# Kernel optimization log

Hardware: AMD Instinct MI355X
Metric: run time of the kernel (lower is better)

## Reference

```python
import jax, jax.numpy as jnp
import numpy as np

B, L, DIM, HEADS, DIM_HEAD = 16, 1024, 512, 8, 64


def _make_perms(rng):
    # perm = identity on first DIM indices, random permutation of [DIM, L*DIM) after
    perms = []
    for _ in range(HEADS - 1):
        tail = rng.permutation(np.arange(DIM, L * DIM))
        perms.append(np.concatenate([np.arange(DIM), tail]))
    return jnp.asarray(np.stack(perms), dtype=jnp.int64)


def setup_inputs() -> dict:
    key = jax.random.key(0)
    ks = jax.random.split(key, 6)
    s = 0.02
    return {
        "x": jax.random.normal(ks[0], (B, L, DIM), dtype=jnp.float32),
        "perms": _make_perms(np.random.default_rng(0)),
        "Wq": jax.random.normal(ks[1], (HEADS, DIM, DIM_HEAD), dtype=jnp.float32) * s,
        "Wk": jax.random.normal(ks[2], (HEADS, DIM, DIM_HEAD), dtype=jnp.float32) * s,
        "Wv": jax.random.normal(ks[3], (HEADS, DIM, DIM_HEAD), dtype=jnp.float32) * s,
        "Wo": jax.random.normal(ks[4], (DIM, HEADS * DIM_HEAD), dtype=jnp.float32) * s,
        "bo": jnp.zeros((DIM,), dtype=jnp.float32),
    }


def reference(x, perms, Wq, Wk, Wv, Wo, bo):
    b, l, d = x.shape
    h, _, e = Wq.shape
    scale = e ** -0.5
    # shuffled query inputs for heads 1..h-1
    flat = x.reshape(b, l * d)                      # [B, L*D]
    shuf = flat[:, perms].reshape(b, h - 1, l, d)   # [B, H-1, L, D]
    xq = jnp.concatenate([x[:, None], shuf], axis=1)  # [B, H, L, D]
    q = jnp.einsum('bhld,hde->bhle', xq, Wq)
    k = jnp.einsum('bld,hde->bhle', x, Wk)
    v = jnp.einsum('bld,hde->bhle', x, Wv)
    attn = jax.nn.softmax(jnp.einsum('bhqe,bhke->bhqk', q, k) * scale, axis=-1)
    out = jnp.einsum('bhqk,bhke->bhqe', attn, v)    # [B, H, L, E]
    out = out.transpose(0, 2, 1, 3).reshape(b, l, h * e)  # concat heads on last dim
    return jnp.einsum('bli,di->bld', out, Wo) + bo
```

## Files before the change

kernel.cpp:

```cpp
#include <hip/hip_runtime.h>

#define LL 1024
#define DD 512
#define HH 8
#define EE 64
#define LDX (LL*DD)
#define BB 16

typedef _Float16 h8 __attribute__((ext_vector_type(8)));
typedef _Float16 h4 __attribute__((ext_vector_type(4)));
typedef float f4 __attribute__((ext_vector_type(4)));
typedef int i4 __attribute__((ext_vector_type(4)));

__device__ __forceinline__ f4 mfma16(h8 a, h8 b, f4 c) {
    return __builtin_amdgcn_mfma_f32_16x16x32_f16(a, b, c, 0, 0, 0);
}

__global__ __launch_bounds__(256) void k_prep(
    const float* __restrict__ x, _Float16* __restrict__ xT)
{
    const int s = blockIdx.x * 256 + threadIdx.x;
    h8 lo, hi;
    #pragma unroll
    for (int b = 0; b < 8; ++b)  lo[b] = (_Float16)x[(size_t)b*LDX + s];
    #pragma unroll
    for (int b = 0; b < 8; ++b)  hi[b] = (_Float16)x[(size_t)(b+8)*LDX + s];
    _Float16* d = xT + (size_t)s * BB;
    *(h8*)d = lo; *(h8*)(d + 8) = hi;
}

__global__ __launch_bounds__(256) void k_x16(
    const float* __restrict__ x, _Float16* __restrict__ x16)
{
    const int i = blockIdx.x * 256 + threadIdx.x;
    f4 v = ((const f4*)x)[i];
    h4 o;
    #pragma unroll
    for (int j = 0; j < 4; ++j) o[j] = (_Float16)v[j];
    *(h4*)(x16 + 4*(size_t)i) = o;
}

__global__ __launch_bounds__(256) void k_wprep(
    const float* __restrict__ Wq, const float* __restrict__ Wk,
    const float* __restrict__ Wv, _Float16* __restrict__ WT)
{
    const int d0 = blockIdx.x * 64;
    const int zz = blockIdx.y;
    const float* src; float sc = 1.f;
    if (zz < 8)       src = Wk + (size_t)zz*DD*EE;
    else if (zz < 16) src = Wv + (size_t)(zz-8)*DD*EE;
    else            { src = Wq + (size_t)(zz-16)*DD*EE; sc = 0.125f; }
    const int t = threadIdx.x;
    const int e = t & 63, dq = t >> 6;
    #pragma unroll
    for (int i = 0; i < 16; ++i) {
        int d = d0 + dq*16 + i;
        WT[(size_t)(zz*64 + e)*DD + d] = (_Float16)(src[(size_t)d*EE + e] * sc);
    }
}

__global__ __launch_bounds__(256) void k_wo16(
    const float* __restrict__ Wo, _Float16* __restrict__ Wo16)
{
    const int i = blockIdx.x * 256 + threadIdx.x;
    f4 v = ((const f4*)Wo)[i];
    #pragma unroll
    for (int j = 0; j < 4; ++j) Wo16[4*i + j] = (_Float16)v[j];
}

__global__ __launch_bounds__(256) void k_qkv(
    const _Float16* __restrict__ x16, const _Float16* __restrict__ WT,
    _Float16* __restrict__ qw, _Float16* __restrict__ kw, _Float16* __restrict__ vw)
{
    const int y  = blockIdx.x;
    const int r0 = blockIdx.y * 128;

    __shared__ __align__(16) _Float16 As[2][128][72];
    __shared__ __align__(16) _Float16 Bs[2][128][72];

    const int t = threadIdx.x;
    const int wv = t >> 6, lane = t & 63;
    const int m = lane & 15, qd = lane >> 4;
    const int sr = t >> 1, sc0 = (t & 1) * 32;

    const _Float16* ax = x16 + (size_t)(r0 + sr)*DD + sc0;
    const _Float16* bx = WT  + (size_t)(y*128 + sr)*DD + sc0;

    #pragma unroll
    for (int c = 0; c < 4; ++c) {
        *(h8*)&As[0][sr][sc0 + 8*c] = *(const h8*)(ax + 8*c);
        *(h8*)&Bs[0][sr][sc0 + 8*c] = *(const h8*)(bx + 8*c);
    }
    __syncthreads();

    f4 acc[2][8] = {};
    int cur = 0;
    for (int kt = 0; kt < 8; ++kt) {
        const int alt = cur ^ 1;
        h8 an[4], bn[4];
        if (kt < 7) {
            const _Float16* a2 = ax + (kt+1)*64;
            const _Float16* b2 = bx + (kt+1)*64;
            #pragma unroll
            for (int c = 0; c < 4; ++c) {
                an[c] = *(const h8*)(a2 + 8*c);
                bn[c] = *(const h8*)(b2 + 8*c);
            }
        }
        #pragma unroll
        for (int ks = 0; ks < 2; ++ks) {
            h8 a0 = *(const h8*)&As[cur][32*wv +  0 + m][32*ks + 8*qd];
            h8 a1 = *(const h8*)&As[cur][32*wv + 16 + m][32*ks + 8*qd];
            #pragma unroll
            for (int nt = 0; nt < 8; ++nt) {
                h8 bb = *(const h8*)&Bs[cur][16*nt + m][32*ks + 8*qd];
                acc[0][nt] = mfma16(a0, bb, acc[0][nt]);
                acc[1][nt] = mfma16(a1, bb, acc[1][nt]);
            }
        }
        if (kt < 7) {
            #pragma unroll
            for (int c = 0; c < 4; ++c) {
                *(h8*)&As[alt][sr][sc0 + 8*c] = an[c];
                *(h8*)&Bs[alt][sr][sc0 + 8*c] = bn[c];
            }
            __syncthreads();
            cur = alt;
        }
    }

    #pragma unroll
    for (int nt = 0; nt < 8; ++nt) {
        const int n = y*128 + 16*nt + m;
        const int z = n >> 6, e = n & 63;
        if (z >= 17) continue;
        _Float16* dst; int h;
        if (z < 8)       { dst = kw; h = z; }
        else if (z < 16) { dst = vw; h = z - 8; }
        else             { dst = qw; h = 0; }
        dst += (size_t)h*LL*EE + e;
        #pragma unroll
        for (int mt = 0; mt < 2; ++mt)
            #pragma unroll
            for (int r = 0; r < 4; ++r) {
                int R = r0 + 32*wv + 16*mt + 4*qd + r;
                int b = R >> 10, l = R & 1023;
                dst[((size_t)b*HH*LL + l)*EE] = (_Float16)acc[mt][nt][r];
            }
    }
}

__global__ __launch_bounds__(256) void k_qshuf(
    const _Float16* __restrict__ xT, const int* __restrict__ perms,
    const _Float16* __restrict__ WT, _Float16* __restrict__ qw)
{
    const int l0 = blockIdx.x * 4;
    const int h  = blockIdx.y + 1;
    const _Float16* Wb = WT + (size_t)((16 + h)*64)*DD;
    const int* pbase = perms + (size_t)(h-1)*LDX;

    __shared__ __align__(16) _Float16 As[2][64][72];
    __shared__ __align__(16) _Float16 Bs[2][64][72];

    const int t = threadIdx.x;
    const int wv = t >> 6, lane = t & 63;
    const int m = lane & 15, qd = lane >> 4;
    const int lg = t >> 6, kcol = t & 63;
    const int br = t >> 2, bc0 = (t & 3) * 16;

    int pv[8];
    #pragma unroll
    for (int kt = 0; kt < 8; ++kt)
        pv[kt] = pbase[(size_t)(l0 + lg)*DD + kt*64 + kcol];

    {
        const _Float16* g = xT + (size_t)pv[0] * BB;
        h8 g0 = *(const h8*)g, g1 = *(const h8*)(g + 8);
        const _Float16* s = Wb + (size_t)br*DD + bc0;
        *(h8*)&Bs[0][br][bc0]     = *(const h8*)s;
        *(h8*)&Bs[0][br][bc0 + 8] = *(const h8*)(s + 8);
        #pragma unroll
        for (int i = 0; i < 8; ++i) As[0][lg*16 + i][kcol]     = g0[i];
        #pragma unroll
        for (int i = 0; i < 8; ++i) As[0][lg*16 + 8 + i][kcol] = g1[i];
    }
    __syncthreads();

    f4 acc[4] = {};
    int cur = 0;
    for (int kt = 0; kt < 8; ++kt) {
        const int alt = cur ^ 1;
        h8 g0n, g1n, b0n, b1n;
        if (kt < 7) {
            const _Float16* g = xT + (size_t)pv[kt+1] * BB;
            g0n = *(const h8*)g; g1n = *(const h8*)(g + 8);
            const _Float16* s = Wb + (size_t)br*DD + (kt+1)*64 + bc0;
            b0n = *(const h8*)s; b1n = *(const h8*)(s + 8);
        }
        #pragma unroll
        for (int ks = 0; ks < 2; ++ks) {
            h8 a = *(const h8*)&As[cur][16*wv + m][32*ks + 8*qd];
            #pragma unroll
            for (int nt = 0; nt < 4; ++nt) {
                h8 bb = *(const h8*)&Bs[cur][16*nt + m][32*ks + 8*qd];
                acc[nt] = mfma16(a, bb, acc[nt]);
            }
        }
        if (kt < 7) {
            *(h8*)&Bs[alt][br][bc0]     = b0n;
            *(h8*)&Bs[alt][br][bc0 + 8] = b1n;
            #pragma unroll
            for (int i = 0; i < 8; ++i) As[alt][lg*16 + i][kcol]     = g0n[i];
            #pragma unroll
            for (int i = 0; i < 8; ++i) As[alt][lg*16 + 8 + i][kcol] = g1n[i];
            __syncthreads();
            cur = alt;
        }
    }
    #pragma unroll
    for (int nt = 0; nt < 4; ++nt)
        #pragma unroll
        for (int r = 0; r < 4; ++r) {
            int b = 4*qd + r;
            qw[((size_t)(b*HH + h)*LL + l0 + wv)*EE + 16*nt + m] = (_Float16)acc[nt][r];
        }
}

__global__ __launch_bounds__(256, 3) void k_attn(
    const _Float16* __restrict__ qw, const _Float16* __restrict__ kw,
    const _Float16* __restrict__ vw, _Float16* __restrict__ oa)
{
    const int bh = blockIdx.x;
    const int l0 = blockIdx.y * 128;
    const int b = bh >> 3, h = bh & 7;
    const _Float16* qb = qw + ((size_t)bh*LL + l0)*EE;
    const _Float16* kb = kw + (size_t)bh*LL*EE;
    const _Float16* vb = vw + (size_t)bh*LL*EE;

    __shared__ __align__(16) _Float16 KsF[2][64*64];
    __shared__ __align__(16) _Float16 VtsF[2][64*64];
    __shared__ __align__(16) _Float16 Ps[128][72];

    const int t = threadIdx.x;
    const int wv = t >> 6, lane = t & 63;
    const int m = lane & 15, qd = lane >> 4;
    const int m7 = m & 7;
    const int krow = t >> 2, c0 = t & 3;
    const int vkey = t & 63, vec = t >> 6;
    const int vhi = vkey >> 3, vlo = vkey & 7;

    h8 qa[2][2];
    #pragma unroll
    for (int mt = 0; mt < 2; ++mt)
        #pragma unroll
        for (int ks = 0; ks < 2; ++ks)
            qa[mt][ks] = *(const h8*)(qb + (size_t)(32*wv + 16*mt + m)*EE + 32*ks + 8*qd);

    f4 oacc[2][4] = {};
    float lp[2][4] = {};

    {
        const _Float16* sk = kb + (size_t)krow*EE + 16*c0;
        h8 k0 = *(const h8*)sk, k1 = *(const h8*)(sk + 8);
        const _Float16* sv = vb + (size_t)vkey*EE + 16*vec;
        h8 v0 = *(const h8*)sv, v1 = *(const h8*)(sv + 8);
        *(h8*)&KsF[0][(krow<<6) + 8*((2*c0)     ^ (krow & 7))] = k0;
        *(h8*)&KsF[0][(krow<<6) + 8*((2*c0 + 1) ^ (krow & 7))] = k1;
        #pragma unroll
        for (int i = 0; i < 8; ++i)
            VtsF[0][((16*vec + i)<<6)     + 8*(vhi ^ i) + vlo] = v0[i];
        #pragma unroll
        for (int i = 0; i < 8; ++i)
            VtsF[0][((16*vec + 8 + i)<<6) + 8*(vhi ^ i) + vlo] = v1[i];
    }
    __syncthreads();

    for (int kt = 0; kt < 16; ++kt) {
        const int cur = kt & 1, alt = cur ^ 1;
        h8 kn0, kn1, vn0, vn1;
        if (kt < 15) {
            const _Float16* sk = kb + (size_t)((kt+1)*64 + krow)*EE + 16*c0;
            kn0 = *(const h8*)sk; kn1 = *(const h8*)(sk + 8);
            const _Float16* sv = vb + (size_t)((kt+1)*64 + vkey)*EE + 16*vec;
            vn0 = *(const h8*)sv; vn1 = *(const h8*)(sv + 8);
        }
        f4 sacc[2][4] = {};
        #pragma unroll
        for (int ks = 0; ks < 2; ++ks)
            #pragma unroll
            for (int nt = 0; nt < 4; ++nt) {
                h8 kf = *(const h8*)&KsF[cur][((16*nt + m)<<6) + 8*((4*ks + qd) ^ m7)];
                sacc[0][nt] = mfma16(qa[0][ks], kf, sacc[0][nt]);
                sacc[1][nt] = mfma16(qa[1][ks], kf, sacc[1][nt]);
            }
        #pragma unroll
        for (int mt = 0; mt < 2; ++mt)
            #pragma unroll
            for (int nt = 0; nt < 4; ++nt)
                #pragma unroll
                for (int r = 0; r < 4; ++r) {
                    float e = __expf(sacc[mt][nt][r]);
                    lp[mt][r] += e;
                    Ps[32*wv + 16*mt + 4*qd + r][16*nt + m] = (_Float16)e;
                }
        #pragma unroll
        for (int ks = 0; ks < 2; ++ks) {
            h8 pa0 = *(const h8*)&Ps[32*wv +  0 + m][32*ks + 8*qd];
            h8 pa1 = *(const h8*)&Ps[32*wv + 16 + m][32*ks + 8*qd];
            #pragma unroll
            for (int nt = 0; nt < 4; ++nt) {
                h8 vf = *(const h8*)&VtsF[cur][((16*nt + m)<<6) + 8*((4*ks + qd) ^ m7)];
                oacc[0][nt] = mfma16(pa0, vf, oacc[0][nt]);
                oacc[1][nt] = mfma16(pa1, vf, oacc[1][nt]);
            }
        }
        if (kt < 15) {
            *(h8*)&KsF[alt][(krow<<6) + 8*((2*c0)     ^ (krow & 7))] = kn0;
            *(h8*)&KsF[alt][(krow<<6) + 8*((2*c0 + 1) ^ (krow & 7))] = kn1;
            #pragma unroll
            for (int i = 0; i < 8; ++i)
                VtsF[alt][((16*vec + i)<<6)     + 8*(vhi ^ i) + vlo] = vn0[i];
            #pragma unroll
            for (int i = 0; i < 8; ++i)
                VtsF[alt][((16*vec + 8 + i)<<6) + 8*(vhi ^ i) + vlo] = vn1[i];
            __syncthreads();
        }
    }

    #pragma unroll
    for (int mt = 0; mt < 2; ++mt)
        #pragma unroll
        for (int r = 0; r < 4; ++r) {
            float s = lp[mt][r];
            s += __shfl_xor(s, 1, 64);
            s += __shfl_xor(s, 2, 64);
            s += __shfl_xor(s, 4, 64);
            s += __shfl_xor(s, 8, 64);
            lp[mt][r] = s;
        }

    _Float16* ob = oa + ((size_t)(b*LL + l0))*(HH*EE) + h*EE;
    #pragma unroll
    for (int mt = 0; mt < 2; ++mt)
        #pragma unroll
        for (int nt = 0; nt < 4; ++nt)
            #pragma unroll
            for (int r = 0; r < 4; ++r) {
                int row = 32*wv + 16*mt + 4*qd + r;
                ob[(size_t)row*(HH*EE) + 16*nt + m] = (_Float16)(oacc[mt][nt][r] / lp[mt][r]);
            }
}

__global__ __launch_bounds__(256) void k_oproj(
    const _Float16* __restrict__ oa, const _Float16* __restrict__ Wo16,
    const float* __restrict__ bo, float* __restrict__ out)
{
    const int y  = blockIdx.x;
    const int r0 = blockIdx.y * 128;

    __shared__ __align__(16) _Float16 As[2][128][72];
    __shared__ __align__(16) _Float16 Bs[2][128][72];

    const int t = threadIdx.x;
    const int wv = t >> 6, lane = t & 63;
    const int m = lane & 15, qd = lane >> 4;
    const int sr = t >> 1, sc0 = (t & 1) * 32;

    const _Float16* ax = oa   + (size_t)(r0 + sr)*DD + sc0;
    const _Float16* bx = Wo16 + (size_t)(y*128 + sr)*DD + sc0;

    #pragma unroll
    for (int c = 0; c < 4; ++c) {
        *(h8*)&As[0][sr][sc0 + 8*c] = *(const h8*)(ax + 8*c);
        *(h8*)&Bs[0][sr][sc0 + 8*c] = *(const h8*)(bx + 8*c);
    }
    __syncthreads();

    f4 acc[2][8] = {};
    int cur = 0;
    for (int kt = 0; kt < 8; ++kt) {
        const int alt = cur ^ 1;
        h8 an[4], bn[4];
        if (kt < 7) {
            const _Float16* a2 = ax + (kt+1)*64;
            const _Float16* b2 = bx + (kt+1)*64;
            #pragma unroll
            for (int c = 0; c < 4; ++c) {
                an[c] = *(const h8*)(a2 + 8*c);
                bn[c] = *(const h8*)(b2 + 8*c);
            }
        }
        #pragma unroll
        for (int ks = 0; ks < 2; ++ks) {
            h8 a0 = *(const h8*)&As[cur][32*wv +  0 + m][32*ks + 8*qd];
            h8 a1 = *(const h8*)&As[cur][32*wv + 16 + m][32*ks + 8*qd];
            #pragma unroll
            for (int nt = 0; nt < 8; ++nt) {
                h8 bb = *(const h8*)&Bs[cur][16*nt + m][32*ks + 8*qd];
                acc[0][nt] = mfma16(a0, bb, acc[0][nt]);
                acc[1][nt] = mfma16(a1, bb, acc[1][nt]);
            }
        }
        if (kt < 7) {
            #pragma unroll
            for (int c = 0; c < 4; ++c) {
                *(h8*)&As[alt][sr][sc0 + 8*c] = an[c];
                *(h8*)&Bs[alt][sr][sc0 + 8*c] = bn[c];
            }
            __syncthreads();
            cur = alt;
        }
    }

    #pragma unroll
    for (int nt = 0; nt < 8; ++nt) {
        const int col = y*128 + 16*nt + m;
        const float bias = bo[col];
        #pragma unroll
        for (int mt = 0; mt < 2; ++mt)
            #pragma unroll
            for (int r = 0; r < 4; ++r) {
                int row = 32*wv + 16*mt + 4*qd + r;
                out[(size_t)(r0 + row)*DD + col] = acc[mt][nt][r] + bias;
            }
    }
}

extern "C" void kernel_launch(void* const* d_in, const int* in_sizes, int n_in,
                              void* d_out, int out_size, void* d_ws, size_t ws_size,
                              hipStream_t stream)
{
    const float* x  = (const float*)d_in[0];
    const int*   pm = (const int*)d_in[1];
    const float* Wq = (const float*)d_in[2];
    const float* Wk = (const float*)d_in[3];
    const float* Wv = (const float*)d_in[4];
    const float* Wo = (const float*)d_in[5];
    const float* bo = (const float*)d_in[6];
    float* out = (float*)d_out;

    const size_t QS = (size_t)BB * HH * LL * EE;
    _Float16* q    = (_Float16*)d_ws;
    _Float16* k    = q + QS;
    _Float16* v    = k + QS;
    _Float16* oaw  = v + QS;
    _Float16* xT   = oaw;
    _Float16* WT   = oaw + QS;
    _Float16* Wo16 = WT + (size_t)24*64*DD;
    _Float16* x16  = (_Float16*)d_out;

    k_x16  <<<dim3(LDX*BB/1024),    256, 0, stream>>>(x, x16);
    k_prep <<<dim3(LDX/256),        256, 0, stream>>>(x, xT);
    k_wprep<<<dim3(8, 24),          256, 0, stream>>>(Wq, Wk, Wv, WT);
    k_wo16 <<<dim3(DD*DD/1024),     256, 0, stream>>>(Wo, Wo16);
    k_qkv  <<<dim3(9, BB*LL/128),   256, 0, stream>>>(x16, WT, q, k, v);
    k_qshuf<<<dim3(LL/4, HH-1),     256, 0, stream>>>(xT, pm, WT, q);
    k_attn <<<dim3(BB*HH, LL/128),  256, 0, stream>>>(q, k, v, oaw);
    k_oproj<<<dim3(DD/128, BB*LL/128), 256, 0, stream>>>(oaw, Wo16, bo, out);
}
```

Before: 290.4 us.

## Use exp2 with folded log2e scale, MFMA row sums, prefetch all gathered rows

Folds log2(e) into the Q weight scale so the attention kernel can use the hardware exp2 directly. The softmax row sums are now computed by extra MFMAs against a ones vector instead of per-element VALU adds and shuffle reductions, and the final division becomes a multiply by the reciprocal. In the Q-projection kernel, all eight gathered xT rows are loaded up front to expose more memory parallelism, at the cost of more registers. The row sums now accumulate from fp16-rounded probabilities rather than fp32 values.

```diff
diff --git a/kernel.cpp b/kernel.cpp
--- a/kernel.cpp
+++ b/kernel.cpp
@@ -49,7 +49,7 @@
     const float* src; float sc = 1.f;
     if (zz < 8)       src = Wk + (size_t)zz*DD*EE;
     else if (zz < 16) src = Wv + (size_t)(zz-8)*DD*EE;
-    else            { src = Wq + (size_t)(zz-16)*DD*EE; sc = 0.125f; }
+    else            { src = Wq + (size_t)(zz-16)*DD*EE; sc = 0.18033688011112042f; }
     const int t = threadIdx.x;
     const int e = t & 63, dq = t >> 6;
     #pragma unroll
@@ -173,16 +173,22 @@
     for (int kt = 0; kt < 8; ++kt)
         pv[kt] = pbase[(size_t)(l0 + lg)*DD + kt*64 + kcol];
 
+    h8 g0[8], g1[8];
+    #pragma unroll
+    for (int kt = 0; kt < 8; ++kt) {
+        const _Float16* g = xT + (size_t)pv[kt] * BB;
+        g0[kt] = *(const h8*)g;
+        g1[kt] = *(const h8*)(g + 8);
+    }
+
     {
-        const _Float16* g = xT + (size_t)pv[0] * BB;
-        h8 g0 = *(const h8*)g, g1 = *(const h8*)(g + 8);
         const _Float16* s = Wb + (size_t)br*DD + bc0;
         *(h8*)&Bs[0][br][bc0]     = *(const h8*)s;
         *(h8*)&Bs[0][br][bc0 + 8] = *(const h8*)(s + 8);
         #pragma unroll
-        for (int i = 0; i < 8; ++i) As[0][lg*16 + i][kcol]     = g0[i];
-        #pragma unroll
-        for (int i = 0; i < 8; ++i) As[0][lg*16 + 8 + i][kcol] = g1[i];
+        for (int i = 0; i < 8; ++i) As[0][lg*16 + i][kcol]     = g0[0][i];
+        #pragma unroll
+        for (int i = 0; i < 8; ++i) As[0][lg*16 + 8 + i][kcol] = g1[0][i];
     }
     __syncthreads();
 
@@ -190,10 +196,8 @@
     int cur = 0;
     for (int kt = 0; kt < 8; ++kt) {
         const int alt = cur ^ 1;
-        h8 g0n, g1n, b0n, b1n;
-        if (kt < 7) {
-            const _Float16* g = xT + (size_t)pv[kt+1] * BB;
-            g0n = *(const h8*)g; g1n = *(const h8*)(g + 8);
+        h8 b0n, b1n;
+        if (kt < 7) {
             const _Float16* s = Wb + (size_t)br*DD + (kt+1)*64 + bc0;
             b0n = *(const h8*)s; b1n = *(const h8*)(s + 8);
         }
@@ -210,9 +214,9 @@
             *(h8*)&Bs[alt][br][bc0]     = b0n;
             *(h8*)&Bs[alt][br][bc0 + 8] = b1n;
             #pragma unroll
-            for (int i = 0; i < 8; ++i) As[alt][lg*16 + i][kcol]     = g0n[i];
-            #pragma unroll
-            for (int i = 0; i < 8; ++i) As[alt][lg*16 + 8 + i][kcol] = g1n[i];
+            for (int i = 0; i < 8; ++i) As[alt][lg*16 + i][kcol]     = g0[kt+1][i];
+            #pragma unroll
+            for (int i = 0; i < 8; ++i) As[alt][lg*16 + 8 + i][kcol] = g1[kt+1][i];
             __syncthreads();
             cur = alt;
         }
@@ -256,8 +260,14 @@
         for (int ks = 0; ks < 2; ++ks)
             qa[mt][ks] = *(const h8*)(qb + (size_t)(32*wv + 16*mt + m)*EE + 32*ks + 8*qd);
 
+    h8 bones = {};
+    if (m == 0) {
+        #pragma unroll
+        for (int i = 0; i < 8; ++i) bones[i] = (_Float16)1.0f;
+    }
+
     f4 oacc[2][4] = {};
-    float lp[2][4] = {};
+    f4 lsacc[2] = {};
 
     {
         const _Float16* sk = kb + (size_t)krow*EE + 16*c0;
@@ -298,11 +308,9 @@
             #pragma unroll
             for (int nt = 0; nt < 4; ++nt)
                 #pragma unroll
-                for (int r = 0; r < 4; ++r) {
-                    float e = __expf(sacc[mt][nt][r]);
-                    lp[mt][r] += e;
-                    Ps[32*wv + 16*mt + 4*qd + r][16*nt + m] = (_Float16)e;
-                }
+                for (int r = 0; r < 4; ++r)
+                    Ps[32*wv + 16*mt + 4*qd + r][16*nt + m] =
+                        (_Float16)__builtin_amdgcn_exp2f(sacc[mt][nt][r]);
         #pragma unroll
         for (int ks = 0; ks < 2; ++ks) {
             h8 pa0 = *(const h8*)&Ps[32*wv +  0 + m][32*ks + 8*qd];
@@ -313,6 +321,8 @@
                 oacc[0][nt] = mfma16(pa0, vf, oacc[0][nt]);
                 oacc[1][nt] = mfma16(pa1, vf, oacc[1][nt]);
             }
+            lsacc[0] = mfma16(pa0, bones, lsacc[0]);
+            lsacc[1] = mfma16(pa1, bones, lsacc[1]);
         }
         if (kt < 15) {
             *(h8*)&KsF[alt][(krow<<6) + 8*((2*c0)     ^ (krow & 7))] = kn0;
@@ -327,17 +337,12 @@
         }
     }
 
+    float inv[2][4];
     #pragma unroll
     for (int mt = 0; mt < 2; ++mt)
         #pragma unroll
-        for (int r = 0; r < 4; ++r) {
-            float s = lp[mt][r];
-            s += __shfl_xor(s, 1, 64);
-            s += __shfl_xor(s, 2, 64);
-            s += __shfl_xor(s, 4, 64);
-            s += __shfl_xor(s, 8, 64);
-            lp[mt][r] = s;
-        }
+        for (int r = 0; r < 4; ++r)
+            inv[mt][r] = 1.0f / __shfl(lsacc[mt][r], lane & 48, 64);
 
     _Float16* ob = oa + ((size_t)(b*LL + l0))*(HH*EE) + h*EE;
     #pragma unroll
@@ -347,7 +352,7 @@
             #pragma unroll
             for (int r = 0; r < 4; ++r) {
                 int row = 32*wv + 16*mt + 4*qd + r;
-                ob[(size_t)row*(HH*EE) + 16*nt + m] = (_Float16)(oacc[mt][nt][r] / lp[mt][r]);
+                ob[(size_t)row*(HH*EE) + 16*nt + m] = (_Float16)(oacc[mt][nt][r] * inv[mt][r]);
             }
 }
 
```

Measured after the change: 294.6 us. About the same (+1.5%).
